# Optimization experiments

Measured on AMD Instinct MI355X. Metric: run time of the kernel, lower is better.

Reference implementation:

```python
import jax, jax.numpy as jnp
import numpy as np

N = 50000   # nodes
E = 800000  # edges (avg degree 16)
IN, HID, OUT = 128, 128, 64


def setup_inputs() -> dict:
    key = jax.random.key(0)
    ks = jax.random.split(key, 8)
    x = jax.random.normal(ks[0], (N, IN), dtype=jnp.float32)
    edge_index = jax.random.randint(ks[1], (2, E), 0, N, dtype=jnp.int32)
    s = 0.05
    W1 = jax.random.normal(ks[2], (IN, HID), dtype=jnp.float32) * s
    b1 = jnp.zeros((HID,), dtype=jnp.float32)
    W2 = jax.random.normal(ks[3], (HID, HID), dtype=jnp.float32) * s
    b2 = jnp.zeros((HID,), dtype=jnp.float32)
    W3 = jax.random.normal(ks[4], (HID, OUT), dtype=jnp.float32) * s
    b3 = jnp.zeros((OUT,), dtype=jnp.float32)
    return {"x": x, "edge_index": edge_index, "W1": W1, "b1": b1,
            "W2": W2, "b2": b2, "W3": W3, "b3": b3}


def _gcn_norm(edge_index, n):
    # PyG GCNConv default: add self-loops, symmetric normalization D^-1/2 A D^-1/2
    loop = jnp.arange(n, dtype=edge_index.dtype)
    src = jnp.concatenate([edge_index[0], loop])  # [E+N]
    dst = jnp.concatenate([edge_index[1], loop])  # [E+N]
    deg = jax.ops.segment_sum(jnp.ones_like(dst, dtype=jnp.float32), dst,
                              num_segments=n)  # degree of destination (col)
    dinv = jax.lax.rsqrt(deg)  # deg >= 1 due to self-loops
    norm = dinv[src] * dinv[dst]  # [E+N]
    return src, dst, norm


def _gcn_conv(x, src, dst, norm, W, b, n):
    h = x @ W                      # [N, F_out]  (transform first, fewer flops)
    msg = h[src] * norm[:, None]   # gather + scale  [E+N, F_out]
    agg = jax.ops.segment_sum(msg, dst, num_segments=n)
    return agg + b


def reference(x, edge_index, W1, b1, W2, b2, W3, b3):
    n = x.shape[0]
    src, dst, norm = _gcn_norm(edge_index, n)
    h = jax.nn.relu(_gcn_conv(x, src, dst, norm, W1, b1, n))
    h = jax.nn.relu(_gcn_conv(h, src, dst, norm, W2, b2, n))
    # dropout p=0.0 / eval mode -> identity
    out = jax.nn.relu(h @ W3 + b3)
    return out
```

## Files before the change

### kernel.cpp

```cpp
#include <hip/hip_runtime.h>
#include <hip/hip_fp16.h>
#include <cstddef>
#include <type_traits>


typedef _Float16 half8 __attribute__((ext_vector_type(8)));
typedef float f32x4 __attribute__((ext_vector_type(4)));

constexpr int CAP = 4608;

__global__ __launch_bounds__(256) void prep(const float* __restrict__ W1,
                                            const float* __restrict__ W2,
                                            const float* __restrict__ W3,
                                            __half* __restrict__ w1t,
                                            __half* __restrict__ w2t,
                                            __half* __restrict__ w3t,
                                            int* __restrict__ gcount, int nb) {
    int b = blockIdx.x;
    if (b == 0 && threadIdx.x < nb) gcount[threadIdx.x] = 0;
    const float* W;
    __half* Wt;
    int ncol, i;
    if (b < 64) { W = W1; Wt = w1t; ncol = 128; i = b * 256 + threadIdx.x; }
    else if (b < 128) { W = W2; Wt = w2t; ncol = 128; i = (b - 64) * 256 + threadIdx.x; }
    else { W = W3; Wt = w3t; ncol = 64; i = (b - 128) * 256 + threadIdx.x; }
    if (i < 128 * ncol) {
        int k = i / ncol, c = i - k * ncol;
        Wt[c * 128 + k] = __float2half(W[i]);
    }
}

__global__ __launch_bounds__(1024) void bucket_p1(const int* __restrict__ src,
                                                  const int* __restrict__ dst,
                                                  int* __restrict__ gcount,
                                                  int2* __restrict__ gbucket,
                                                  int nb, int e) {
    __shared__ int lcnt[256];
    __shared__ int lbase[256];
    int t = threadIdx.x;
    if (t < nb) lcnt[t] = 0;
    __syncthreads();

    int base = blockIdx.x * 8192 + t * 8;
    int d[8], s[8], pb[8], pp[8];
    if (base + 8 <= e) {
        *(int4*)&d[0] = *(const int4*)&dst[base];
        *(int4*)&d[4] = *(const int4*)&dst[base + 4];
        *(int4*)&s[0] = *(const int4*)&src[base];
        *(int4*)&s[4] = *(const int4*)&src[base + 4];
    } else {
#pragma unroll
        for (int u = 0; u < 8; ++u) {
            d[u] = (base + u < e) ? dst[base + u] : -1;
            s[u] = (base + u < e) ? src[base + u] : 0;
        }
    }
#pragma unroll
    for (int u = 0; u < 8; ++u) {
        if (d[u] >= 0) {
            pb[u] = d[u] >> 8;
            pp[u] = atomicAdd(&lcnt[pb[u]], 1);
        }
    }
    __syncthreads();
    if (t < nb) lbase[t] = lcnt[t] ? atomicAdd(&gcount[t], lcnt[t]) : 0;
    __syncthreads();
#pragma unroll
    for (int u = 0; u < 8; ++u) {
        if (d[u] >= 0) {
            int p = lbase[pb[u]] + pp[u];
            if (p < CAP) gbucket[(size_t)pb[u] * CAP + p] = make_int2(d[u], s[u]);
        }
    }
}

__device__ __forceinline__ void gemm_tile_xf32(const float* __restrict__ A,
                                               const __half* __restrict__ Wt,
                                               __half* __restrict__ C, int M,
                                               int tile, int t) {
    constexpr int NC = 4;
    const int w = t >> 6, l = t & 63;
    const int lr = l & 15, kg = l >> 4;
    const int rh = w >> 1, ch = w & 1;
    const int r0 = tile * 64 + rh * 32;

    half8 wf[NC][4];
#pragma unroll
    for (int c = 0; c < NC; ++c)
#pragma unroll
        for (int ks = 0; ks < 4; ++ks)
            wf[c][ks] = *(const half8*)&Wt[(size_t)((ch * NC + c) * 16 + lr) * 128 +
                                           ks * 32 + kg * 8];

    f32x4 acc[2][NC];
#pragma unroll
    for (int rt = 0; rt < 2; ++rt)
#pragma unroll
        for (int c = 0; c < NC; ++c) acc[rt][c] = (f32x4){0.f, 0.f, 0.f, 0.f};

    const int row0 = r0 + lr, row1 = r0 + 16 + lr;
    const bool ok0 = row0 < M, ok1 = row1 < M;
#pragma unroll
    for (int ks = 0; ks < 4; ++ks) {
        half8 af0 = (half8)(_Float16)0, af1 = (half8)(_Float16)0;
        if (ok0) {
            float4 p = *(const float4*)&A[(size_t)row0 * 128 + ks * 32 + kg * 8];
            float4 q = *(const float4*)&A[(size_t)row0 * 128 + ks * 32 + kg * 8 + 4];
            af0[0] = (_Float16)p.x; af0[1] = (_Float16)p.y;
            af0[2] = (_Float16)p.z; af0[3] = (_Float16)p.w;
            af0[4] = (_Float16)q.x; af0[5] = (_Float16)q.y;
            af0[6] = (_Float16)q.z; af0[7] = (_Float16)q.w;
        }
        if (ok1) {
            float4 p = *(const float4*)&A[(size_t)row1 * 128 + ks * 32 + kg * 8];
            float4 q = *(const float4*)&A[(size_t)row1 * 128 + ks * 32 + kg * 8 + 4];
            af1[0] = (_Float16)p.x; af1[1] = (_Float16)p.y;
            af1[2] = (_Float16)p.z; af1[3] = (_Float16)p.w;
            af1[4] = (_Float16)q.x; af1[5] = (_Float16)q.y;
            af1[6] = (_Float16)q.z; af1[7] = (_Float16)q.w;
        }
#pragma unroll
        for (int c = 0; c < NC; ++c) {
            acc[0][c] = __builtin_amdgcn_mfma_f32_16x16x32_f16(wf[c][ks], af0, acc[0][c], 0, 0, 0);
            acc[1][c] = __builtin_amdgcn_mfma_f32_16x16x32_f16(wf[c][ks], af1, acc[1][c], 0, 0, 0);
        }
    }

#pragma unroll
    for (int rt = 0; rt < 2; ++rt) {
        int row = r0 + rt * 16 + lr;
        if (row < M) {
#pragma unroll
            for (int c = 0; c < NC; ++c) {
                int col = (ch * NC + c) * 16 + kg * 4;
                __half2 p0 = __floats2half2_rn(acc[rt][c][0], acc[rt][c][1]);
                __half2 p1 = __floats2half2_rn(acc[rt][c][2], acc[rt][c][3]);
                *(int2*)&C[(size_t)row * 128 + col] = make_int2(*(int*)&p0, *(int*)&p1);
            }
        }
    }
}

__global__ __launch_bounds__(256) void build_and_g1(const int* __restrict__ gcount,
                                                    const int2* __restrict__ gbucket,
                                                    int* __restrict__ offs,
                                                    float* __restrict__ dinv,
                                                    int* __restrict__ eidx,
                                                    const float* __restrict__ x,
                                                    const __half* __restrict__ w1t,
                                                    __half* __restrict__ g1buf,
                                                    int n, int nb) {
    __shared__ int srcS[CAP];
    __shared__ int sc[256];
    __shared__ int cur[256];
    const int bid = blockIdx.x, t = threadIdx.x;

    if (bid >= nb) {
        gemm_tile_xf32(x, w1t, g1buf, n, bid - nb, t);
        return;
    }

    int node0 = bid << 8;
    int own = (t < nb) ? gcount[t] : 0;
    sc[t] = own;
    __syncthreads();
    for (int d = 1; d < 256; d <<= 1) {
        int u = (t >= d) ? sc[t - d] : 0;
        __syncthreads();
        sc[t] += u;
        __syncthreads();
    }
    cur[t] = sc[t] - own;
    if (bid == 0 && t == 0) offs[n] = sc[255];
    __syncthreads();
    int gb = cur[bid];
    int cnt = min(gcount[bid], CAP);
    __syncthreads();

    cur[t] = 0;
    __syncthreads();
    const int2* gbp = gbucket + (size_t)bid * CAP;
    for (int i = t; i < cnt; i += 256) {
        int2 pr = gbp[i];
        atomicAdd(&cur[pr.x - node0], 1);
    }
    __syncthreads();
    own = cur[t];
    sc[t] = own;
    __syncthreads();
    for (int d = 1; d < 256; d <<= 1) {
        int u = (t >= d) ? sc[t - d] : 0;
        __syncthreads();
        sc[t] += u;
        __syncthreads();
    }
    int excl = sc[t] - own;
    int node = node0 + t;
    if (node < n) {
        offs[node] = gb + excl;
        dinv[node] = rsqrtf((float)(own + 1));
    }
    cur[t] = excl;
    __syncthreads();
    for (int i = t; i < cnt; i += 256) {
        int2 pr = gbp[i];
        int pos = atomicAdd(&cur[pr.x - node0], 1);
        srcS[pos] = pr.y;
    }
    __syncthreads();
    for (int i = t; i < cnt; i += 256) eidx[gb + i] = srcS[i];
}

template <int N2, bool EPI, typename OT, bool IN_PRE, bool OUT_PRE>
__global__ __launch_bounds__(256) void agg_gemm(const __half* __restrict__ g,
                                                const float* __restrict__ dinv,
                                                const int* __restrict__ offs,
                                                const int* __restrict__ eidx,
                                                const float* __restrict__ biasA,
                                                const __half* __restrict__ Wt,
                                                const float* __restrict__ biasG,
                                                OT* __restrict__ C, int n) {
    __shared__ alignas(16) char hs[16 * 256];
    const int t = threadIdx.x;
    const int node0 = blockIdx.x * 16;
    constexpr int UN = IN_PRE ? 16 : 8;

    {
        int row = t >> 4;
        int lane = t & 15;
        int node = node0 + row;
        int bo = (lane * 16) ^ ((row & 7) << 4);
        if (node < n) {
            const int4* h4 = (const int4*)g;
            float dv = dinv[node];
            int4 sp = h4[(size_t)node * 16 + lane];
            float a0, a1, a2, a3, a4, a5, a6, a7;
            {
                float nm = IN_PRE ? 1.f : dv * dv;
                float2 f0 = __half22float2(*(__half2*)&sp.x);
                float2 f1 = __half22float2(*(__half2*)&sp.y);
                float2 f2 = __half22float2(*(__half2*)&sp.z);
                float2 f3 = __half22float2(*(__half2*)&sp.w);
                a0 = f0.x * nm; a1 = f0.y * nm; a2 = f1.x * nm; a3 = f1.y * nm;
                a4 = f2.x * nm; a5 = f2.y * nm; a6 = f3.x * nm; a7 = f3.y * nm;
            }
            int beg = offs[node], end = offs[node + 1];
            int j = beg;
            for (; j + UN <= end; j += UN) {
                int s[UN];
                float wg[UN];
                int4 hv[UN];
#pragma unroll
                for (int u = 0; u < UN; ++u) s[u] = eidx[j + u];
#pragma unroll
                for (int u = 0; u < UN; ++u) {
                    if constexpr (!IN_PRE) wg[u] = dinv[s[u]];
                    hv[u] = h4[(size_t)s[u] * 16 + lane];
                }
#pragma unroll
                for (int u = 0; u < UN; ++u) {
                    float2 g0 = __half22float2(*(__half2*)&hv[u].x);
                    float2 g1 = __half22float2(*(__half2*)&hv[u].y);
                    float2 g2 = __half22float2(*(__half2*)&hv[u].z);
                    float2 g3 = __half22float2(*(__half2*)&hv[u].w);
                    if constexpr (IN_PRE) {
                        a0 += g0.x; a1 += g0.y; a2 += g1.x; a3 += g1.y;
                        a4 += g2.x; a5 += g2.y; a6 += g3.x; a7 += g3.y;
                    } else {
                        float wu = wg[u] * dv;
                        a0 = fmaf(g0.x, wu, a0); a1 = fmaf(g0.y, wu, a1);
                        a2 = fmaf(g1.x, wu, a2); a3 = fmaf(g1.y, wu, a3);
                        a4 = fmaf(g2.x, wu, a4); a5 = fmaf(g2.y, wu, a5);
                        a6 = fmaf(g3.x, wu, a6); a7 = fmaf(g3.y, wu, a7);
                    }
                }
            }
            if (j < end) {
                int s[UN];
                float wg[UN];
                int4 hv[UN];
#pragma unroll
                for (int u = 0; u < UN; ++u) {
                    int idx = j + u;
                    s[u] = eidx[idx < end ? idx : end - 1];
                }
#pragma unroll
                for (int u = 0; u < UN; ++u) {
                    if constexpr (IN_PRE) wg[u] = (j + u < end) ? 1.f : 0.f;
                    else                  wg[u] = (j + u < end) ? dinv[s[u]] : 0.f;
                    hv[u] = h4[(size_t)s[u] * 16 + lane];
                }
#pragma unroll
                for (int u = 0; u < UN; ++u) {
                    float wu = IN_PRE ? wg[u] : wg[u] * dv;
                    float2 g0 = __half22float2(*(__half2*)&hv[u].x);
                    float2 g1 = __half22float2(*(__half2*)&hv[u].y);
                    float2 g2 = __half22float2(*(__half2*)&hv[u].z);
                    float2 g3 = __half22float2(*(__half2*)&hv[u].w);
                    a0 = fmaf(g0.x, wu, a0); a1 = fmaf(g0.y, wu, a1);
                    a2 = fmaf(g1.x, wu, a2); a3 = fmaf(g1.y, wu, a3);
                    a4 = fmaf(g2.x, wu, a4); a5 = fmaf(g2.y, wu, a5);
                    a6 = fmaf(g3.x, wu, a6); a7 = fmaf(g3.y, wu, a7);
                }
            }
            if constexpr (IN_PRE) {
                a0 *= dv; a1 *= dv; a2 *= dv; a3 *= dv;
                a4 *= dv; a5 *= dv; a6 *= dv; a7 *= dv;
            }
            float4 b0 = *(const float4*)&biasA[lane * 8];
            float4 b1 = *(const float4*)&biasA[lane * 8 + 4];
            a0 = fmaxf(a0 + b0.x, 0.f); a1 = fmaxf(a1 + b0.y, 0.f);
            a2 = fmaxf(a2 + b0.z, 0.f); a3 = fmaxf(a3 + b0.w, 0.f);
            a4 = fmaxf(a4 + b1.x, 0.f); a5 = fmaxf(a5 + b1.y, 0.f);
            a6 = fmaxf(a6 + b1.z, 0.f); a7 = fmaxf(a7 + b1.w, 0.f);
            __half2 o0 = __floats2half2_rn(a0, a1);
            __half2 o1 = __floats2half2_rn(a2, a3);
            __half2 o2 = __floats2half2_rn(a4, a5);
            __half2 o3 = __floats2half2_rn(a6, a7);
            *(int4*)&hs[row * 256 + bo] =
                make_int4(*(int*)&o0, *(int*)&o1, *(int*)&o2, *(int*)&o3);
        } else {
            *(int4*)&hs[row * 256 + bo] = make_int4(0, 0, 0, 0);
        }
    }
    __syncthreads();

    constexpr int NW = N2 / 4;
    constexpr int NC = NW / 16;
    const int w = t >> 6, l = t & 63;
    const int lr = l & 15, kg = l >> 4;

    half8 wf[NC][4];
#pragma unroll
    for (int c = 0; c < NC; ++c)
#pragma unroll
        for (int ks = 0; ks < 4; ++ks)
            wf[c][ks] = *(const half8*)&Wt[(size_t)(w * NW + c * 16 + lr) * 128 +
                                           ks * 32 + kg * 8];

    half8 af[4];
#pragma unroll
    for (int ks = 0; ks < 4; ++ks) {
        int bo = (ks * 64 + kg * 16) ^ ((lr & 7) << 4);
        af[ks] = *(const half8*)&hs[lr * 256 + bo];
    }

    f32x4 acc[NC];
#pragma unroll
    for (int c = 0; c < NC; ++c) acc[c] = (f32x4){0.f, 0.f, 0.f, 0.f};
#pragma unroll
    for (int ks = 0; ks < 4; ++ks)
#pragma unroll
        for (int c = 0; c < NC; ++c)
            acc[c] = __builtin_amdgcn_mfma_f32_16x16x32_f16(wf[c][ks], af[ks], acc[c], 0, 0, 0);

    int row = node0 + lr;
    if (row < n) {
        float dvr = OUT_PRE ? dinv[row] : 1.f;
#pragma unroll
        for (int c = 0; c < NC; ++c) {
            int col = w * NW + c * 16 + kg * 4;
            float v0 = acc[c][0], v1 = acc[c][1], v2 = acc[c][2], v3 = acc[c][3];
            if constexpr (EPI) {
                float4 bv = *(const float4*)&biasG[col];
                v0 = fmaxf(v0 + bv.x, 0.f);
                v1 = fmaxf(v1 + bv.y, 0.f);
                v2 = fmaxf(v2 + bv.z, 0.f);
                v3 = fmaxf(v3 + bv.w, 0.f);
            }
            if constexpr (OUT_PRE) { v0 *= dvr; v1 *= dvr; v2 *= dvr; v3 *= dvr; }
            if constexpr (std::is_same_v<OT, float>) {
                *(float4*)&C[(size_t)row * N2 + col] = make_float4(v0, v1, v2, v3);
            } else {
                __half2 p0 = __floats2half2_rn(v0, v1);
                __half2 p1 = __floats2half2_rn(v2, v3);
                *(int2*)&C[(size_t)row * N2 + col] = make_int2(*(int*)&p0, *(int*)&p1);
            }
        }
    }
}

extern "C" void kernel_launch(void* const* d_in, const int* in_sizes, int n_in,
                              void* d_out, int out_size, void* d_ws, size_t ws_size,
                              hipStream_t stream) {
    const float* x  = (const float*)d_in[0];
    const int* ei   = (const int*)d_in[1];
    const float* W1 = (const float*)d_in[2];
    const float* b1 = (const float*)d_in[3];
    const float* W2 = (const float*)d_in[4];
    const float* b2 = (const float*)d_in[5];
    const float* W3 = (const float*)d_in[6];
    const float* b3 = (const float*)d_in[7];
    float* out = (float*)d_out;

    const int N = in_sizes[0] / 128;
    const int E = in_sizes[1] / 2;
    const int* esrc = ei;
    const int* edst = ei + E;
    const int nb = (N + 255) >> 8;

    char* w = (char*)d_ws;
    size_t off = 0;
    auto alloc = [&](size_t bytes) {
        void* p = w + off;
        off = (off + bytes + 255) & ~(size_t)255;
        return p;
    };
    int*    gcount  = (int*)alloc((size_t)nb * 4);
    int2*   gbucket = (int2*)alloc((size_t)nb * CAP * 8);
    int*    offs    = (int*)alloc((size_t)(N + 1) * 4);
    float*  dinv    = (float*)alloc((size_t)N * 4);
    int*    eidx    = (int*)alloc((size_t)E * 4);
    __half* w1t     = (__half*)alloc(128 * 128 * 2);
    __half* w2t     = (__half*)alloc(128 * 128 * 2);
    __half* w3t     = (__half*)alloc(64 * 128 * 2);
    __half* g1buf   = (__half*)alloc((size_t)N * 128 * 2);
    __half* g2buf   = (__half*)alloc((size_t)N * 128 * 2);
    (void)ws_size;

    const int gemm_blocks = (N + 63) / 64;
    const int agg_blocks = (N + 15) / 16;

    prep<<<160, 256, 0, stream>>>(W1, W2, W3, w1t, w2t, w3t, gcount, nb);
    bucket_p1<<<(E + 8191) / 8192, 1024, 0, stream>>>(esrc, edst, gcount, gbucket, nb, E);
    build_and_g1<<<nb + gemm_blocks, 256, 0, stream>>>(gcount, gbucket, offs, dinv,
                                                       eidx, x, w1t, g1buf, N, nb);
    agg_gemm<128, false, __half, false, true><<<agg_blocks, 256, 0, stream>>>(
        g1buf, dinv, offs, eidx, b1, w2t, nullptr, g2buf, N);
    agg_gemm<64, true, float, true, false><<<agg_blocks, 256, 0, stream>>>(
        g2buf, dinv, offs, eidx, b2, w3t, b3, out, N);
}
```

Baseline: 115.0 us.

## Overlap edge bucketing with first GEMM and pack bucket entries into one int

Moves the layer-1 feature GEMM out of the CSR build kernel and into the edge-bucketing kernel, so the GEMM overlaps with bucketing instead of with the build. The build now runs as a small separate kernel. Bucketing blocks shrink from 1024 to 256 threads, giving more, smaller blocks. Bucket entries are packed as (src<<8 | dst&255) into a single int, which halves bucket memory traffic but assumes node indices fit in 24 bits.

```diff
diff --git a/kernel.cpp b/kernel.cpp
--- a/kernel.cpp
+++ b/kernel.cpp
@@ -30,50 +30,6 @@
     }
 }
 
-__global__ __launch_bounds__(1024) void bucket_p1(const int* __restrict__ src,
-                                                  const int* __restrict__ dst,
-                                                  int* __restrict__ gcount,
-                                                  int2* __restrict__ gbucket,
-                                                  int nb, int e) {
-    __shared__ int lcnt[256];
-    __shared__ int lbase[256];
-    int t = threadIdx.x;
-    if (t < nb) lcnt[t] = 0;
-    __syncthreads();
-
-    int base = blockIdx.x * 8192 + t * 8;
-    int d[8], s[8], pb[8], pp[8];
-    if (base + 8 <= e) {
-        *(int4*)&d[0] = *(const int4*)&dst[base];
-        *(int4*)&d[4] = *(const int4*)&dst[base + 4];
-        *(int4*)&s[0] = *(const int4*)&src[base];
-        *(int4*)&s[4] = *(const int4*)&src[base + 4];
-    } else {
-#pragma unroll
-        for (int u = 0; u < 8; ++u) {
-            d[u] = (base + u < e) ? dst[base + u] : -1;
-            s[u] = (base + u < e) ? src[base + u] : 0;
-        }
-    }
-#pragma unroll
-    for (int u = 0; u < 8; ++u) {
-        if (d[u] >= 0) {
-            pb[u] = d[u] >> 8;
-            pp[u] = atomicAdd(&lcnt[pb[u]], 1);
-        }
-    }
-    __syncthreads();
-    if (t < nb) lbase[t] = lcnt[t] ? atomicAdd(&gcount[t], lcnt[t]) : 0;
-    __syncthreads();
-#pragma unroll
-    for (int u = 0; u < 8; ++u) {
-        if (d[u] >= 0) {
-            int p = lbase[pb[u]] + pp[u];
-            if (p < CAP) gbucket[(size_t)pb[u] * CAP + p] = make_int2(d[u], s[u]);
-        }
-    }
-}
-
 __device__ __forceinline__ void gemm_tile_xf32(const float* __restrict__ A,
                                                const __half* __restrict__ Wt,
                                                __half* __restrict__ C, int M,
@@ -141,26 +97,69 @@
     }
 }
 
-__global__ __launch_bounds__(256) void build_and_g1(const int* __restrict__ gcount,
-                                                    const int2* __restrict__ gbucket,
-                                                    int* __restrict__ offs,
-                                                    float* __restrict__ dinv,
-                                                    int* __restrict__ eidx,
-                                                    const float* __restrict__ x,
-                                                    const __half* __restrict__ w1t,
-                                                    __half* __restrict__ g1buf,
-                                                    int n, int nb) {
+__global__ __launch_bounds__(256) void bucket_and_g1(const int* __restrict__ src,
+                                                     const int* __restrict__ dst,
+                                                     int* __restrict__ gcount,
+                                                     int* __restrict__ gbucket,
+                                                     int nb, int e, int nbkt,
+                                                     const float* __restrict__ x,
+                                                     const __half* __restrict__ w1t,
+                                                     __half* __restrict__ g1buf, int n) {
+    const int bid = blockIdx.x, t = threadIdx.x;
+    if (bid >= nbkt) {
+        gemm_tile_xf32(x, w1t, g1buf, n, bid - nbkt, t);
+        return;
+    }
+    __shared__ int lcnt[256];
+    __shared__ int lbase[256];
+    if (t < nb) lcnt[t] = 0;
+    __syncthreads();
+
+    int base = bid * 2048 + t * 8;
+    int d[8], s[8], pb[8], pp[8];
+    if (base + 8 <= e) {
+        *(int4*)&d[0] = *(const int4*)&dst[base];
+        *(int4*)&d[4] = *(const int4*)&dst[base + 4];
+        *(int4*)&s[0] = *(const int4*)&src[base];
+        *(int4*)&s[4] = *(const int4*)&src[base + 4];
+    } else {
+#pragma unroll
+        for (int u = 0; u < 8; ++u) {
+            d[u] = (base + u < e) ? dst[base + u] : -1;
+            s[u] = (base + u < e) ? src[base + u] : 0;
+        }
+    }
+#pragma unroll
+    for (int u = 0; u < 8; ++u) {
+        if (d[u] >= 0) {
+            pb[u] = d[u] >> 8;
+            pp[u] = atomicAdd(&lcnt[pb[u]], 1);
+        }
+    }
+    __syncthreads();
+    if (t < nb) lbase[t] = lcnt[t] ? atomicAdd(&gcount[t], lcnt[t]) : 0;
+    __syncthreads();
+#pragma unroll
+    for (int u = 0; u < 8; ++u) {
+        if (d[u] >= 0) {
+            int p = lbase[pb[u]] + pp[u];
+            if (p < CAP)
+                gbucket[(size_t)pb[u] * CAP + p] = (s[u] << 8) | (d[u] & 255);
+        }
+    }
+}
+
+__global__ __launch_bounds__(256) void build_p2(const int* __restrict__ gcount,
+                                                const int* __restrict__ gbucket,
+                                                int* __restrict__ offs,
+                                                float* __restrict__ dinv,
+                                                int* __restrict__ eidx, int n, int nb) {
     __shared__ int srcS[CAP];
     __shared__ int sc[256];
     __shared__ int cur[256];
     const int bid = blockIdx.x, t = threadIdx.x;
-
-    if (bid >= nb) {
-        gemm_tile_xf32(x, w1t, g1buf, n, bid - nb, t);
-        return;
-    }
-
     int node0 = bid << 8;
+
     int own = (t < nb) ? gcount[t] : 0;
     sc[t] = own;
     __syncthreads();
@@ -179,11 +178,8 @@
 
     cur[t] = 0;
     __syncthreads();
-    const int2* gbp = gbucket + (size_t)bid * CAP;
-    for (int i = t; i < cnt; i += 256) {
-        int2 pr = gbp[i];
-        atomicAdd(&cur[pr.x - node0], 1);
-    }
+    const int* gbp = gbucket + (size_t)bid * CAP;
+    for (int i = t; i < cnt; i += 256) atomicAdd(&cur[gbp[i] & 255], 1);
     __syncthreads();
     own = cur[t];
     sc[t] = own;
@@ -203,9 +199,9 @@
     cur[t] = excl;
     __syncthreads();
     for (int i = t; i < cnt; i += 256) {
-        int2 pr = gbp[i];
-        int pos = atomicAdd(&cur[pr.x - node0], 1);
-        srcS[pos] = pr.y;
+        int pr = gbp[i];
+        int pos = atomicAdd(&cur[pr & 255], 1);
+        srcS[pos] = pr >> 8;
     }
     __syncthreads();
     for (int i = t; i < cnt; i += 256) eidx[gb + i] = srcS[i];
@@ -407,7 +403,7 @@
         return p;
     };
     int*    gcount  = (int*)alloc((size_t)nb * 4);
-    int2*   gbucket = (int2*)alloc((size_t)nb * CAP * 8);
+    int*    gbucket = (int*)alloc((size_t)nb * CAP * 4);
     int*    offs    = (int*)alloc((size_t)(N + 1) * 4);
     float*  dinv    = (float*)alloc((size_t)N * 4);
     int*    eidx    = (int*)alloc((size_t)E * 4);
@@ -419,12 +415,13 @@
     (void)ws_size;
 
     const int gemm_blocks = (N + 63) / 64;
+    const int nbkt = (E + 2047) / 2048;
     const int agg_blocks = (N + 15) / 16;
 
     prep<<<160, 256, 0, stream>>>(W1, W2, W3, w1t, w2t, w3t, gcount, nb);
-    bucket_p1<<<(E + 8191) / 8192, 1024, 0, stream>>>(esrc, edst, gcount, gbucket, nb, E);
-    build_and_g1<<<nb + gemm_blocks, 256, 0, stream>>>(gcount, gbucket, offs, dinv,
-                                                       eidx, x, w1t, g1buf, N, nb);
+    bucket_and_g1<<<nbkt + gemm_blocks, 256, 0, stream>>>(
+        esrc, edst, gcount, gbucket, nb, E, nbkt, x, w1t, g1buf, N);
+    build_p2<<<nb, 256, 0, stream>>>(gcount, gbucket, offs, dinv, eidx, N, nb);
     agg_gemm<128, false, __half, false, true><<<agg_blocks, 256, 0, stream>>>(
         g1buf, dinv, offs, eidx, b1, w2t, nullptr, g2buf, N);
     agg_gemm<64, true, float, true, false><<<agg_blocks, 256, 0, stream>>>(
```

Result: slower. 121.2 us (+5.5%).
